# Optimization experiments

Measured on AMD Instinct MI355X. Metric: run time of the kernel, lower is better.

## Reference

```python
import jax, jax.numpy as jnp
import numpy as np

S, B, C = 7, 2, 20
D = C + 5 * B  # 30
LAMBDA_COORD = 5.0
LAMBDA_NOOBJ = 0.5
EPS = 1e-6


def _iou_yolo(b1, b2):
    # b1, b2: [..., 4] boxes in (cx, cy, w, h) 'yolo' format
    b1x1 = b1[..., 0] - b1[..., 2] / 2
    b1y1 = b1[..., 1] - b1[..., 3] / 2
    b1x2 = b1[..., 0] + b1[..., 2] / 2
    b1y2 = b1[..., 1] + b1[..., 3] / 2
    b2x1 = b2[..., 0] - b2[..., 2] / 2
    b2y1 = b2[..., 1] - b2[..., 3] / 2
    b2x2 = b2[..., 0] + b2[..., 2] / 2
    b2y2 = b2[..., 1] + b2[..., 3] / 2
    iw = jnp.clip(jnp.minimum(b1x2, b2x2) - jnp.maximum(b1x1, b2x1), 0.0)
    ih = jnp.clip(jnp.minimum(b1y2, b2y2) - jnp.maximum(b1y1, b2y1), 0.0)
    inter = iw * ih
    a1 = jnp.abs((b1x2 - b1x1) * (b1y2 - b1y1))
    a2 = jnp.abs((b2x2 - b2x1) * (b2y2 - b2y1))
    return inter / (a1 + a2 - inter + EPS)


def setup_inputs() -> dict:
    batch = 16384
    key = jax.random.key(0)
    k1, k2, k3 = jax.random.split(key, 3)
    # true coords / classes in (0.05, 0.95) so sqrt(w), sqrt(h) are well-defined
    y_trues = jax.random.uniform(k1, (batch, S, S, D), dtype=jnp.float32) * 0.9 + 0.05
    conf = (jax.random.uniform(k2, (batch, S, S)) < 0.3).astype(jnp.float32)
    y_trues = y_trues.at[..., 4].set(conf)  # objectness indicator is exactly 0 or 1
    y_preds = jax.random.normal(k3, (batch, S, S, D), dtype=jnp.float32)
    return {"y_trues": y_trues, "y_preds": y_preds}


def reference(y_trues, y_preds):
    yt = y_trues.reshape(-1, S * S, D)
    yp = y_preds.reshape(-1, S * S, D)
    batch = yt.shape[0]

    obj = (yt[..., 4] == 1.0).astype(yt.dtype)   # [N, S*S]
    noobj = 1.0 - obj

    iou1 = _iou_yolo(yt[..., 0:4], yp[..., 0:4])
    iou2 = _iou_yolo(yt[..., 0:4], yp[..., 5:9])
    best1 = iou1 > iou2                           # responsible box selection

    box_hat = jnp.where(best1[..., None], yp[..., 0:4], yp[..., 5:9])
    conf_hat = jnp.where(best1, yp[..., 4], yp[..., 9])        # responsible conf
    other_conf_hat = jnp.where(best1, yp[..., 9], yp[..., 4])  # non-responsible conf

    # xy offset loss
    xy = (yt[..., 0] - box_hat[..., 0]) ** 2 + (yt[..., 1] - box_hat[..., 1]) ** 2
    # wh loss: sqrt(true) vs sqrt(|pred + eps|)
    wh = (jnp.sqrt(yt[..., 2]) - jnp.sqrt(jnp.abs(box_hat[..., 2] + EPS))) ** 2 \
       + (jnp.sqrt(yt[..., 3]) - jnp.sqrt(jnp.abs(box_hat[..., 3] + EPS))) ** 2
    # object confidence loss (true conf == 1 in obj cells)
    obj_conf = (yt[..., 4] - conf_hat) ** 2
    # no-object penalty on the NON-responsible box inside object cells (target 0)
    noobj_in_obj = LAMBDA_NOOBJ * other_conf_hat ** 2
    # no-object penalty on BOTH boxes in cells without objects (true conf == 0)
    noobj_cells = LAMBDA_NOOBJ * ((yt[..., 4] - yp[..., 4]) ** 2
                                  + (yt[..., 4] - yp[..., 9]) ** 2)
    # class loss over C classes
    cls = jnp.sum((yt[..., 10:] - yp[..., 10:]) ** 2, axis=-1)

    per_cell = obj * (LAMBDA_COORD * (xy + wh) + obj_conf + noobj_in_obj + cls) \
             + noobj * noobj_cells
    return jnp.sum(per_cell) / batch
```

## Files before the change

kernel.cpp:

```cpp
#include <hip/hip_runtime.h>


#define SS 49
#define DD 30

__device__ __forceinline__ float iou_yolo(const float b1[4], const float b2[4]) {
    const float EPS = 1e-6f;
    float b1x1 = b1[0] - b1[2] * 0.5f, b1y1 = b1[1] - b1[3] * 0.5f;
    float b1x2 = b1[0] + b1[2] * 0.5f, b1y2 = b1[1] + b1[3] * 0.5f;
    float b2x1 = b2[0] - b2[2] * 0.5f, b2y1 = b2[1] - b2[3] * 0.5f;
    float b2x2 = b2[0] + b2[2] * 0.5f, b2y2 = b2[1] + b2[3] * 0.5f;
    float iw = fmaxf(fminf(b1x2, b2x2) - fmaxf(b1x1, b2x1), 0.0f);
    float ih = fmaxf(fminf(b1y2, b2y2) - fmaxf(b1y1, b2y1), 0.0f);
    float inter = iw * ih;
    float a1 = fabsf((b1x2 - b1x1) * (b1y2 - b1y1));
    float a2 = fabsf((b2x2 - b2x1) * (b2y2 - b2y1));
    return inter / (a1 + a2 - inter + EPS);
}

__global__ __launch_bounds__(256)
void yolo_loss_kernel(const float* __restrict__ yt_g,
                      const float* __restrict__ yp_g,
                      float* __restrict__ out,
                      int ncells, float inv_batch) {
    const float LAMBDA_COORD = 5.0f;
    const float LAMBDA_NOOBJ = 0.5f;
    const float EPS = 1e-6f;

    int cell = blockIdx.x * blockDim.x + threadIdx.x;
    float per_cell = 0.0f;

    if (cell < ncells) {
        const float2* yt2 = reinterpret_cast<const float2*>(yt_g + (size_t)cell * DD);
        const float2* yp2 = reinterpret_cast<const float2*>(yp_g + (size_t)cell * DD);
        float yt[DD], yp[DD];
#pragma unroll
        for (int i = 0; i < DD / 2; ++i) {
            float2 a = yt2[i]; yt[2 * i] = a.x; yt[2 * i + 1] = a.y;
            float2 b = yp2[i]; yp[2 * i] = b.x; yp[2 * i + 1] = b.y;
        }

        float obj = (yt[4] == 1.0f) ? 1.0f : 0.0f;
        float noobj = 1.0f - obj;

        float iou1 = iou_yolo(&yt[0], &yp[0]);
        float iou2 = iou_yolo(&yt[0], &yp[5]);
        bool best1 = iou1 > iou2;

        float bh0 = best1 ? yp[0] : yp[5];
        float bh1 = best1 ? yp[1] : yp[6];
        float bh2 = best1 ? yp[2] : yp[7];
        float bh3 = best1 ? yp[3] : yp[8];
        float conf_hat       = best1 ? yp[4] : yp[9];
        float other_conf_hat = best1 ? yp[9] : yp[4];

        float dx = yt[0] - bh0, dy = yt[1] - bh1;
        float xy = dx * dx + dy * dy;

        float sw = sqrtf(yt[2]) - sqrtf(fabsf(bh2 + EPS));
        float sh = sqrtf(yt[3]) - sqrtf(fabsf(bh3 + EPS));
        float wh = sw * sw + sh * sh;

        float dc = yt[4] - conf_hat;
        float obj_conf = dc * dc;

        float noobj_in_obj = LAMBDA_NOOBJ * other_conf_hat * other_conf_hat;

        float d4 = yt[4] - yp[4];
        float d9 = yt[4] - yp[9];
        float noobj_cells = LAMBDA_NOOBJ * (d4 * d4 + d9 * d9);

        float cls = 0.0f;
#pragma unroll
        for (int k = 10; k < DD; ++k) {
            float d = yt[k] - yp[k];
            cls += d * d;
        }

        per_cell = obj * (LAMBDA_COORD * (xy + wh) + obj_conf + noobj_in_obj + cls)
                 + noobj * noobj_cells;
    }

#pragma unroll
    for (int off = 32; off > 0; off >>= 1)
        per_cell += __shfl_down(per_cell, off, 64);

    __shared__ float smem[4];
    int lane = threadIdx.x & 63;
    int wave = threadIdx.x >> 6;
    if (lane == 0) smem[wave] = per_cell;
    __syncthreads();
    if (threadIdx.x == 0) {
        float s = smem[0] + smem[1] + smem[2] + smem[3];
        atomicAdd(out, s * inv_batch);
    }
}

extern "C" void kernel_launch(void* const* d_in, const int* in_sizes, int n_in,
                              void* d_out, int out_size, void* d_ws, size_t ws_size,
                              hipStream_t stream) {
    const float* yt = (const float*)d_in[0];
    const float* yp = (const float*)d_in[1];
    float* out = (float*)d_out;

    int total = in_sizes[0];
    int ncells = total / DD;
    int batch = ncells / SS;

    hipMemsetAsync(out, 0, sizeof(float), stream);

    int block = 256;
    int grid = (ncells + block - 1) / block;
    yolo_loss_kernel<<<grid, block, 0, stream>>>(yt, yp, out, ncells, 1.0f / (float)batch);
}
```

Baseline: 212.3 us.

## Stage inputs through shared memory with coalesced float4 loads

Each block now copies its 256 cells of y_trues into LDS using coalesced float4 loads, reads each cell's values from LDS into registers, then does the same for y_preds. The old code had each thread load its own 120-byte cell with strided float2 reads, which coalesce poorly. The new scheme adds two extra barriers and LDS traffic, and the stride-30 LDS reads may cause bank conflicts. The tail handling relies on total being divisible by 4.

```diff
diff --git a/kernel.cpp b/kernel.cpp
--- a/kernel.cpp
+++ b/kernel.cpp
@@ -3,56 +3,83 @@
 
 #define SS 49
 #define DD 30
-
-__device__ __forceinline__ float iou_yolo(const float b1[4], const float b2[4]) {
-    const float EPS = 1e-6f;
-    float b1x1 = b1[0] - b1[2] * 0.5f, b1y1 = b1[1] - b1[3] * 0.5f;
-    float b1x2 = b1[0] + b1[2] * 0.5f, b1y2 = b1[1] + b1[3] * 0.5f;
-    float b2x1 = b2[0] - b2[2] * 0.5f, b2y1 = b2[1] - b2[3] * 0.5f;
-    float b2x2 = b2[0] + b2[2] * 0.5f, b2y2 = b2[1] + b2[3] * 0.5f;
-    float iw = fmaxf(fminf(b1x2, b2x2) - fmaxf(b1x1, b2x1), 0.0f);
-    float ih = fmaxf(fminf(b1y2, b2y2) - fmaxf(b1y1, b2y1), 0.0f);
-    float inter = iw * ih;
-    float a1 = fabsf((b1x2 - b1x1) * (b1y2 - b1y1));
-    float a2 = fabsf((b2x2 - b2x1) * (b2y2 - b2y1));
-    return inter / (a1 + a2 - inter + EPS);
-}
+#define CPB 256
+#define F4B (CPB * DD / 4)
 
 __global__ __launch_bounds__(256)
-void yolo_loss_kernel(const float* __restrict__ yt_g,
-                      const float* __restrict__ yp_g,
+void yolo_loss_kernel(const float4* __restrict__ yt4,
+                      const float4* __restrict__ yp4,
                       float* __restrict__ out,
-                      int ncells, float inv_batch) {
+                      int nf4_total, int ncells, float inv_batch) {
     const float LAMBDA_COORD = 5.0f;
     const float LAMBDA_NOOBJ = 0.5f;
     const float EPS = 1e-6f;
 
-    int cell = blockIdx.x * blockDim.x + threadIdx.x;
+    __shared__ float4 sbuf4[F4B];
+    float* sbuf = reinterpret_cast<float*>(sbuf4);
+
+    const int tid = threadIdx.x;
+    const int f4base = blockIdx.x * F4B;
+    const int cell = blockIdx.x * CPB + tid;
+    const bool valid = cell < ncells;
+
+#pragma unroll
+    for (int k = 0; k < 8; ++k) {
+        int i = tid + k * 256;
+        if (i < F4B && f4base + i < nf4_total) sbuf4[i] = yt4[f4base + i];
+    }
+    __syncthreads();
+
+    float yt[DD];
+    if (valid) {
+#pragma unroll
+        for (int k = 0; k < DD; ++k) yt[k] = sbuf[tid * DD + k];
+    }
+    __syncthreads();
+
+#pragma unroll
+    for (int k = 0; k < 8; ++k) {
+        int i = tid + k * 256;
+        if (i < F4B && f4base + i < nf4_total) sbuf4[i] = yp4[f4base + i];
+    }
+    __syncthreads();
+
     float per_cell = 0.0f;
-
-    if (cell < ncells) {
-        const float2* yt2 = reinterpret_cast<const float2*>(yt_g + (size_t)cell * DD);
-        const float2* yp2 = reinterpret_cast<const float2*>(yp_g + (size_t)cell * DD);
-        float yt[DD], yp[DD];
-#pragma unroll
-        for (int i = 0; i < DD / 2; ++i) {
-            float2 a = yt2[i]; yt[2 * i] = a.x; yt[2 * i + 1] = a.y;
-            float2 b = yp2[i]; yp[2 * i] = b.x; yp[2 * i + 1] = b.y;
-        }
+    if (valid) {
+        const float* yp = &sbuf[tid * DD];
+        float p0 = yp[0], p1 = yp[1], p2 = yp[2], p3 = yp[3], p4 = yp[4];
+        float p5 = yp[5], p6 = yp[6], p7 = yp[7], p8 = yp[8], p9 = yp[9];
 
         float obj = (yt[4] == 1.0f) ? 1.0f : 0.0f;
         float noobj = 1.0f - obj;
 
-        float iou1 = iou_yolo(&yt[0], &yp[0]);
-        float iou2 = iou_yolo(&yt[0], &yp[5]);
+        float tx1 = yt[0] - yt[2] * 0.5f, ty1 = yt[1] - yt[3] * 0.5f;
+        float tx2 = yt[0] + yt[2] * 0.5f, ty2 = yt[1] + yt[3] * 0.5f;
+        float ta = fabsf((tx2 - tx1) * (ty2 - ty1));
+
+        float ax1 = p0 - p2 * 0.5f, ay1 = p1 - p3 * 0.5f;
+        float ax2 = p0 + p2 * 0.5f, ay2 = p1 + p3 * 0.5f;
+        float iw1 = fmaxf(fminf(tx2, ax2) - fmaxf(tx1, ax1), 0.0f);
+        float ih1 = fmaxf(fminf(ty2, ay2) - fmaxf(ty1, ay1), 0.0f);
+        float inter1 = iw1 * ih1;
+        float aa = fabsf((ax2 - ax1) * (ay2 - ay1));
+        float iou1 = inter1 / (ta + aa - inter1 + EPS);
+
+        float bx1 = p5 - p7 * 0.5f, by1 = p6 - p8 * 0.5f;
+        float bx2 = p5 + p7 * 0.5f, by2 = p6 + p8 * 0.5f;
+        float iw2 = fmaxf(fminf(tx2, bx2) - fmaxf(tx1, bx1), 0.0f);
+        float ih2 = fmaxf(fminf(ty2, by2) - fmaxf(ty1, by1), 0.0f);
+        float inter2 = iw2 * ih2;
+        float ba = fabsf((bx2 - bx1) * (by2 - by1));
+        float iou2 = inter2 / (ta + ba - inter2 + EPS);
+
         bool best1 = iou1 > iou2;
-
-        float bh0 = best1 ? yp[0] : yp[5];
-        float bh1 = best1 ? yp[1] : yp[6];
-        float bh2 = best1 ? yp[2] : yp[7];
-        float bh3 = best1 ? yp[3] : yp[8];
-        float conf_hat       = best1 ? yp[4] : yp[9];
-        float other_conf_hat = best1 ? yp[9] : yp[4];
+        float bh0 = best1 ? p0 : p5;
+        float bh1 = best1 ? p1 : p6;
+        float bh2 = best1 ? p2 : p7;
+        float bh3 = best1 ? p3 : p8;
+        float conf_hat       = best1 ? p4 : p9;
+        float other_conf_hat = best1 ? p9 : p4;
 
         float dx = yt[0] - bh0, dy = yt[1] - bh1;
         float xy = dx * dx + dy * dy;
@@ -66,8 +93,8 @@
 
         float noobj_in_obj = LAMBDA_NOOBJ * other_conf_hat * other_conf_hat;
 
-        float d4 = yt[4] - yp[4];
-        float d9 = yt[4] - yp[9];
+        float d4 = yt[4] - p4;
+        float d9 = yt[4] - p9;
         float noobj_cells = LAMBDA_NOOBJ * (d4 * d4 + d9 * d9);
 
         float cls = 0.0f;
@@ -85,13 +112,13 @@
     for (int off = 32; off > 0; off >>= 1)
         per_cell += __shfl_down(per_cell, off, 64);
 
-    __shared__ float smem[4];
-    int lane = threadIdx.x & 63;
-    int wave = threadIdx.x >> 6;
-    if (lane == 0) smem[wave] = per_cell;
+    __shared__ float wsum[4];
+    int lane = tid & 63;
+    int wave = tid >> 6;
+    if (lane == 0) wsum[wave] = per_cell;
     __syncthreads();
-    if (threadIdx.x == 0) {
-        float s = smem[0] + smem[1] + smem[2] + smem[3];
+    if (tid == 0) {
+        float s = wsum[0] + wsum[1] + wsum[2] + wsum[3];
         atomicAdd(out, s * inv_batch);
     }
 }
@@ -99,17 +126,18 @@
 extern "C" void kernel_launch(void* const* d_in, const int* in_sizes, int n_in,
                               void* d_out, int out_size, void* d_ws, size_t ws_size,
                               hipStream_t stream) {
-    const float* yt = (const float*)d_in[0];
-    const float* yp = (const float*)d_in[1];
+    const float4* yt4 = (const float4*)d_in[0];
+    const float4* yp4 = (const float4*)d_in[1];
     float* out = (float*)d_out;
 
     int total = in_sizes[0];
     int ncells = total / DD;
     int batch = ncells / SS;
+    int nf4 = total / 4;
 
     hipMemsetAsync(out, 0, sizeof(float), stream);
 
-    int block = 256;
-    int grid = (ncells + block - 1) / block;
-    yolo_loss_kernel<<<grid, block, 0, stream>>>(yt, yp, out, ncells, 1.0f / (float)batch);
+    int grid = (ncells + CPB - 1) / CPB;
+    yolo_loss_kernel<<<grid, CPB, 0, stream>>>(yt4, yp4, out, nf4, ncells,
+                                               1.0f / (float)batch);
 }
```

Result: slower. 224.4 us (+5.7%).
